# Performance work log

Measured on AMD Instinct MI355X. Metric: run time of the kernel, lower is better.

## Reference

```python
import jax, jax.numpy as jnp
import numpy as np

B, T, D, F, H = 512, 48, 128, 16, 512


def setup_inputs() -> dict:
    key = jax.random.key(0)
    ks = jax.random.split(key, 7)
    return {
        "input": jax.random.normal(ks[0], (B, T, D, F), dtype=jnp.float32),
        "attn_w": jax.random.normal(ks[1], (2 * H + F * T,), dtype=jnp.float32) * 0.02,
        "attn_b": jax.random.normal(ks[2], (1,), dtype=jnp.float32) * 0.02,
        "w_ih": jax.random.normal(ks[3], (4 * H, D * F), dtype=jnp.float32) * 0.02,
        "w_hh": jax.random.normal(ks[4], (4 * H, H), dtype=jnp.float32) * 0.02,
        "b_ih": jax.random.normal(ks[5], (4 * H,), dtype=jnp.float32) * 0.02,
        "b_hh": jax.random.normal(ks[6], (4 * H,), dtype=jnp.float32) * 0.02,
    }


def reference(input, attn_w, attn_b, w_ih, w_hh, b_ih, b_hh):
    Bsz, Ts, Dn, Fn = input.shape
    Hs = w_hh.shape[1]
    # permute(0,2,3,1): [B, T, D, F] -> [B, D, F, T]
    x_perm = jnp.transpose(input, (0, 2, 3, 1))
    x_flat = x_perm.reshape(Bsz, Dn, Fn * Ts)  # [B, D, F*T]
    # encode_attn input is concat(hidden, cell, x); split the weight accordingly
    w_h, w_c, w_x = attn_w[:Hs], attn_w[Hs:2 * Hs], attn_w[2 * Hs:]
    # x contribution to attention logits is constant across steps
    e_x = x_flat @ w_x + attn_b[0]             # [B, D]
    xs = jnp.moveaxis(x_perm, 3, 0)            # [T, B, D, F] (time-major for scan)
    bias = b_ih + b_hh                         # fuse the two LSTM biases

    def step(carry, x_t):
        h, c = carry                           # [B, H] each
        e = e_x + (h @ w_h)[:, None] + (c @ w_c)[:, None]  # [B, D]
        a = jax.nn.softmax(e, axis=-1)
        x_hat = (a[:, :, None] * x_t).reshape(Bsz, Dn * Fn)  # [B, D*F]
        gates = x_hat @ w_ih.T + h @ w_hh.T + bias            # [B, 4H]
        i, f, g, o = jnp.split(gates, 4, axis=-1)  # torch LSTM gate order
        c_new = jax.nn.sigmoid(f) * c + jax.nn.sigmoid(i) * jnp.tanh(g)
        h_new = jax.nn.sigmoid(o) * jnp.tanh(c_new)
        return (h_new, c_new), h_new

    h0 = jnp.zeros((Bsz, Hs), dtype=input.dtype)
    _, hs = jax.lax.scan(step, (h0, h0), xs)   # hs: [T, B, H]
    return jnp.transpose(hs, (1, 0, 2))        # [B, T, H] == hidden_states[:, 1:]
```

## Files before the change

kernel.cpp:

```cpp
#include <hip/hip_runtime.h>

#define B_ 512
#define T_ 48
#define D_ 128
#define F_ 16
#define H_ 512

typedef float f32x4 __attribute__((ext_vector_type(4)));
typedef short s16x8 __attribute__((ext_vector_type(8)));
typedef unsigned short u16x8 __attribute__((ext_vector_type(8)));
typedef unsigned short u16x4 __attribute__((ext_vector_type(4)));
typedef unsigned long long u64;

__device__ __forceinline__ unsigned short f2bf(float x) {
  unsigned u = __float_as_uint(x);
  u += 0x7fffu + ((u >> 16) & 1u);
  return (unsigned short)(u >> 16);
}
__device__ __forceinline__ float bf2f(unsigned short h) {
  return __uint_as_float(((unsigned)h) << 16);
}
__device__ __forceinline__ float sigmoidf_(float x) {
  return 1.f / (1.f + expf(-x));
}

__device__ __forceinline__ void st_sys_u64(u64* p, u64 v) {
  __hip_atomic_store(p, v, __ATOMIC_RELAXED, __HIP_MEMORY_SCOPE_SYSTEM);
}
__device__ __forceinline__ u64 ld_sys_u64(const u64* p) {
  return __hip_atomic_load((u64*)p, __ATOMIC_RELAXED, __HIP_MEMORY_SCOPE_SYSTEM);
}
__device__ __forceinline__ void st_sys_u32(unsigned* p, unsigned v) {
  __hip_atomic_store(p, v, __ATOMIC_RELAXED, __HIP_MEMORY_SCOPE_SYSTEM);
}
__device__ __forceinline__ unsigned ld_sys_u32(const unsigned* p) {
  return __hip_atomic_load((unsigned*)p, __ATOMIC_RELAXED, __HIP_MEMORY_SCOPE_SYSTEM);
}

#define AS1 __attribute__((address_space(1)))
#define AS3 __attribute__((address_space(3)))
__device__ __forceinline__ void g2lds16(const void* g, void* l) {
  __builtin_amdgcn_global_load_lds((const AS1 void*)g, (AS3 void*)l, 16, 0, 0);
}

__global__ __launch_bounds__(256) void k_prep(const float* __restrict__ wih,
                                              const float* __restrict__ whh,
                                              unsigned short* __restrict__ wih_b,
                                              unsigned short* __restrict__ whh_b) {
  long i4 = ((long)blockIdx.x * 256 + threadIdx.x) * 4;
  if (i4 < 4194304) {
    float4 v = *(const float4*)(wih + i4);
    u16x4 o = {f2bf(v.x), f2bf(v.y), f2bf(v.z), f2bf(v.w)};
    *(u16x4*)(wih_b + i4) = o;
  } else {
    long j = i4 - 4194304;
    if (j < 1048576) {
      float4 v = *(const float4*)(whh + j);
      u16x4 o = {f2bf(v.x), f2bf(v.y), f2bf(v.z), f2bf(v.w)};
      *(u16x4*)(whh_b + j) = o;
    }
  }
}

__global__ __launch_bounds__(128) void k_ex(const float* __restrict__ in,
                                            const float* __restrict__ attn_w,
                                            const float* __restrict__ attn_b,
                                            float* __restrict__ a_out) {
  __shared__ float wx[768];
  __shared__ float red[128];
  const int b = blockIdx.x, d = threadIdx.x;
  for (int i = d; i < 768; i += 128) wx[i] = attn_w[1024 + i];
  __syncthreads();
  const float* base = in + (long)b * 98304 + (long)d * 16;
  float acc = 0.f;
  for (int t = 0; t < 48; ++t) {
    const float4* p = (const float4*)(base + (long)t * 2048);
    float4 v0 = p[0], v1 = p[1], v2 = p[2], v3 = p[3];
    acc += v0.x * wx[t]       + v0.y * wx[48 + t]  + v0.z * wx[96 + t]  + v0.w * wx[144 + t];
    acc += v1.x * wx[192 + t] + v1.y * wx[240 + t] + v1.z * wx[288 + t] + v1.w * wx[336 + t];
    acc += v2.x * wx[384 + t] + v2.y * wx[432 + t] + v2.z * wx[480 + t] + v2.w * wx[528 + t];
    acc += v3.x * wx[576 + t] + v3.y * wx[624 + t] + v3.z * wx[672 + t] + v3.w * wx[720 + t];
  }
  acc += attn_b[0];
  red[d] = acc;
  __syncthreads();
  for (int s = 64; s > 0; s >>= 1) {
    if (d < s) red[d] = fmaxf(red[d], red[d + s]);
    __syncthreads();
  }
  float mx = red[0];
  __syncthreads();
  float ex = expf(acc - mx);
  red[d] = ex;
  __syncthreads();
  for (int s = 64; s > 0; s >>= 1) {
    if (d < s) red[d] += red[d + s];
    __syncthreads();
  }
  a_out[b * 128 + d] = ex / red[0];
}

__global__ __launch_bounds__(256) void k_xhat(const float* __restrict__ in,
                                              const float* __restrict__ a,
                                              unsigned short* __restrict__ xh) {
  const int mrow = blockIdx.x;
  const int t = mrow >> 9, b = mrow & 511;
  const int tid = threadIdx.x;
  const int k = tid * 8;
  const int d = k >> 4;
  const int f0 = k & 15;
  const float* src = in + (((long)(b * 48 + t) * 128 + d) * 16 + f0);
  float4 v0 = *(const float4*)src;
  float4 v1 = *(const float4*)(src + 4);
  float s = a[b * 128 + d];
  u16x8 o;
  o[0] = f2bf(v0.x * s); o[1] = f2bf(v0.y * s); o[2] = f2bf(v0.z * s); o[3] = f2bf(v0.w * s);
  o[4] = f2bf(v1.x * s); o[5] = f2bf(v1.y * s); o[6] = f2bf(v1.z * s); o[7] = f2bf(v1.w * s);
  *(u16x8*)(xh + (long)mrow * 2048 + k) = o;
}


#define G_STAGE(ktv, s)                                                         \
  do {                                                                          \
    const long ko_ = (long)(ktv) * 64 + (long)(s) * 262144;                     \
    char* la_ = (char*)SM + ((ktv) & 1) * 32768 + (s) * 16384 + ldsw;           \
    g2lds16(Ag + ko_, la_);                                                     \
    g2lds16(Ag + ko_ + 131072, la_ + 8192);                                     \
    g2lds16(Bg + ko_, la_ + 65536);                                             \
    g2lds16(Bg + ko_ + 131072, la_ + 73728);                                    \
  } while (0)

#define G_LDA(bufel, ksv, mh)                                                   \
  do {                                                                          \
    const unsigned short* ab_ =                                                 \
        SM + (bufel) + aBase + (mh) * 4096 + (psw ^ ((ksv) * 32));              \
    af[0] = *(const s16x8*)(ab_);                                               \
    af[1] = *(const s16x8*)(ab_ + 1024);                                        \
    af[2] = *(const s16x8*)(ab_ + 2048);                                        \
    af[3] = *(const s16x8*)(ab_ + 3072);                                        \
  } while (0)

#define G_LDB(bufel, ksv)                                                       \
  do {                                                                          \
    const unsigned short* bb_ = SM + (bufel) + bBase + (psw ^ ((ksv) * 32));    \
    bv[0] = *(const s16x8*)(bb_);                                               \
    bv[1] = *(const s16x8*)(bb_ + 1024);                                        \
    bv[2] = *(const s16x8*)(bb_ + 2048);                                        \
    bv[3] = *(const s16x8*)(bb_ + 3072);                                        \
  } while (0)

#define G_BARW()                                                                \
  do {                                                                          \
    __builtin_amdgcn_s_barrier();                                               \
    asm volatile("s_waitcnt lgkmcnt(0)" ::: "memory");                          \
    __builtin_amdgcn_sched_barrier(0);                                          \
  } while (0)

#define G_MMA(mh)                                                               \
  do {                                                                          \
    __builtin_amdgcn_s_setprio(1);                                              \
    _Pragma("unroll") for (int mt_ = 0; mt_ < 4; ++mt_)                         \
        _Pragma("unroll") for (int nt_ = 0; nt_ < 4; ++nt_)                     \
            acc[(mh) * 4 + mt_][nt_] = __builtin_amdgcn_mfma_f32_16x16x32_bf16( \
                af[mt_], bv[nt_], acc[(mh) * 4 + mt_][nt_], 0, 0, 0);           \
    __builtin_amdgcn_s_setprio(0);                                              \
  } while (0)

#define G_GATE(n) asm volatile("s_waitcnt vmcnt(" #n ")" ::: "memory")

__global__ __launch_bounds__(512, 2) void k_gemm(const unsigned short* __restrict__ A,
                                                 const unsigned short* __restrict__ Bw,
                                                 unsigned short* __restrict__ C) {
  __shared__ __align__(16) unsigned short SM[65536];
  const int tid = threadIdx.x;
  const int w = tid >> 6, lane = tid & 63;
  const int q = lane >> 4, l16 = lane & 15;
  const int wm = w >> 2, wn = w & 3;
  const int id = blockIdx.x;
  const int xcd = id & 7, j = id >> 3;
  const long m0 = ((long)xcd * 12 + (j >> 3)) * 256;
  const long n0 = (long)(j & 7) * 256;

  const int srow = w * 8 + (lane >> 3);
  const int csrc = (lane & 7) ^ (lane >> 3);
  const unsigned short* Ag = A + (m0 + srow) * 2048 + csrc * 8;
  const unsigned short* Bg = Bw + (n0 + srow) * 2048 + csrc * 8;
  const int ldsw = w * 1024;

  const int psw = (q ^ (l16 & 7)) * 8;
  const int aBase = (wm * 128 + l16) * 64;
  const int bBase = 32768 + (wn * 64 + l16) * 64;

  f32x4 acc[8][4];
  const f32x4 zz = {0.f, 0.f, 0.f, 0.f};
#pragma unroll
  for (int i = 0; i < 8; ++i)
#pragma unroll
    for (int j2 = 0; j2 < 4; ++j2) acc[i][j2] = zz;
  s16x8 af[4], bv[4];

  G_STAGE(0, 0);
  G_STAGE(0, 1);
  G_GATE(0);
  __builtin_amdgcn_s_barrier();

#pragma unroll 2
  for (int kt = 0; kt < 31; ++kt) {
    const int bufel = (kt & 1) * 16384;
    G_LDB(bufel, 0); G_LDA(bufel, 0, 0);
    G_STAGE(kt + 1, 0);
    G_BARW(); G_MMA(0);
    __builtin_amdgcn_s_barrier();
    G_LDA(bufel, 0, 1);
    G_STAGE(kt + 1, 1);
    G_BARW(); G_MMA(1);
    __builtin_amdgcn_s_barrier();
    G_LDB(bufel, 1); G_LDA(bufel, 1, 0);
    G_BARW(); G_MMA(0);
    __builtin_amdgcn_s_barrier();
    G_LDA(bufel, 1, 1);
    G_BARW(); G_MMA(1);
    G_GATE(0);
    __builtin_amdgcn_s_barrier();
  }
  {
    G_LDB(16384, 0); G_LDA(16384, 0, 0);
    G_BARW(); G_MMA(0);
    __builtin_amdgcn_s_barrier();
    G_LDA(16384, 0, 1);
    G_BARW(); G_MMA(1);
    __builtin_amdgcn_s_barrier();
    G_LDB(16384, 1); G_LDA(16384, 1, 0);
    G_BARW(); G_MMA(0);
    __builtin_amdgcn_s_barrier();
    G_LDA(16384, 1, 1);
    G_BARW(); G_MMA(1);
  }

#pragma unroll
  for (int mh = 0; mh < 2; ++mh)
#pragma unroll
    for (int mt = 0; mt < 4; ++mt)
#pragma unroll
      for (int nt = 0; nt < 4; ++nt)
#pragma unroll
        for (int r = 0; r < 4; ++r) {
          long m = m0 + wm * 128 + mh * 64 + mt * 16 + q * 4 + r;
          long n = n0 + wn * 64 + nt * 16 + l16;
          C[m * 2048 + n] = f2bf(acc[mh * 4 + mt][nt][r]);
        }
}

__global__ __launch_bounds__(256, 1) void k_rec(const unsigned short* __restrict__ gx,
                                                const unsigned short* __restrict__ whh_b,
                                                const float* __restrict__ b_ih,
                                                const float* __restrict__ b_hh,
                                                unsigned short* __restrict__ h_buf,
                                                float* __restrict__ out,
                                                unsigned int* __restrict__ bar) {
  __shared__ unsigned short hs[32 * 528];
  __shared__ float gsm[4 * 32 * 36];
  const int tid = threadIdx.x;
  const int wave = tid >> 6, lane = tid & 63;
  const int q = lane >> 4, l16 = lane & 15;
  const int bt = blockIdx.x & 15, g = blockIdx.x >> 4;
  const int b0 = bt * 32;
  const int pm = tid >> 3, pr = (tid & 7) * 4;
  const int srow = tid >> 3, st7 = tid & 7;
  unsigned int* slots = &bar[bt * 16];

  s16x8 wreg[32];
#pragma unroll
  for (int nt = 0; nt < 2; ++nt) {
    const unsigned short* wp = whh_b + (long)(wave * 512 + g * 32 + nt * 16 + l16) * 512 + q * 8;
#pragma unroll
    for (int kk = 0; kk < 16; ++kk)
      wreg[nt * 16 + kk] = *(const s16x8*)(wp + kk * 32);
  }
#pragma unroll
  for (int i = 0; i < 32; ++i) asm volatile("" : "+v"(wreg[i]));

  float bias_[16];
#pragma unroll
  for (int qq = 0; qq < 4; ++qq)
#pragma unroll
    for (int rr = 0; rr < 4; ++rr) {
      int j = qq * 512 + g * 32 + pr + rr;
      bias_[qq * 4 + rr] = b_ih[j] + b_hh[j];
    }
  float creg[4] = {0.f, 0.f, 0.f, 0.f};
  const f32x4 zz = {0.f, 0.f, 0.f, 0.f};

  for (int t = 0; t < 48; ++t) {
    u16x4 gxr[4];
    const unsigned short* gp = gx + ((long)t * 512 + b0 + pm) * 2048 + g * 32 + pr;
#pragma unroll
    for (int qq = 0; qq < 4; ++qq) gxr[qq] = *(const u16x4*)(gp + qq * 512);

    f32x4 acc[2][2] = {{zz, zz}, {zz, zz}};
    if (t > 0) {
      if (wave == 0 && lane < 16) {
        while (ld_sys_u32(&slots[lane]) < (unsigned)t)
          __builtin_amdgcn_s_sleep(1);
      }
      __syncthreads();
      const u64* hp = (const u64*)(h_buf + ((t - 1) & 1) * (512 * 512) + (long)b0 * 512);
      u64 tmp[16];
#pragma unroll
      for (int j = 0; j < 16; ++j)
        tmp[j] = ld_sys_u64(hp + (long)srow * 128 + st7 + 8 * j);
#pragma unroll
      for (int j = 0; j < 16; ++j)
        *(u64*)&hs[srow * 528 + (st7 + 8 * j) * 4] = tmp[j];
      __syncthreads();
#pragma unroll
      for (int kk = 0; kk < 16; ++kk) {
        s16x8 af0 = *(const s16x8*)&hs[l16 * 528 + kk * 32 + q * 8];
        s16x8 af1 = *(const s16x8*)&hs[(16 + l16) * 528 + kk * 32 + q * 8];
        acc[0][0] = __builtin_amdgcn_mfma_f32_16x16x32_bf16(af0, wreg[kk],      acc[0][0], 0, 0, 0);
        acc[0][1] = __builtin_amdgcn_mfma_f32_16x16x32_bf16(af0, wreg[16 + kk], acc[0][1], 0, 0, 0);
        acc[1][0] = __builtin_amdgcn_mfma_f32_16x16x32_bf16(af1, wreg[kk],      acc[1][0], 0, 0, 0);
        acc[1][1] = __builtin_amdgcn_mfma_f32_16x16x32_bf16(af1, wreg[16 + kk], acc[1][1], 0, 0, 0);
      }
    }
#pragma unroll
    for (int mt = 0; mt < 2; ++mt)
#pragma unroll
      for (int nt = 0; nt < 2; ++nt)
        *(f32x4*)&gsm[(wave * 32 + nt * 16 + l16) * 36 + mt * 16 + q * 4] = acc[mt][nt];
    __syncthreads();
    float hval[4];
#pragma unroll
    for (int rr = 0; rr < 4; ++rr) {
      float gv[4];
#pragma unroll
      for (int qq = 0; qq < 4; ++qq)
        gv[qq] = gsm[(qq * 32 + pr + rr) * 36 + pm] + bf2f(gxr[qq][rr]) + bias_[qq * 4 + rr];
      float is = sigmoidf_(gv[0]);
      float fs = sigmoidf_(gv[1]);
      float gt = tanhf(gv[2]);
      float os = sigmoidf_(gv[3]);
      creg[rr] = fs * creg[rr] + is * gt;
      hval[rr] = os * tanhf(creg[rr]);
    }
    u16x4 hb = {f2bf(hval[0]), f2bf(hval[1]), f2bf(hval[2]), f2bf(hval[3])};
    u64 hb8;
    __builtin_memcpy(&hb8, &hb, 8);
    st_sys_u64((u64*)&h_buf[(t & 1) * (512 * 512) + (b0 + pm) * 512 + g * 32 + pr], hb8);
    f32x4 ov = {hval[0], hval[1], hval[2], hval[3]};
    __builtin_nontemporal_store(ov, (f32x4*)&out[(long)(b0 + pm) * (T_ * H_) + (long)t * H_ + g * 32 + pr]);
    __syncthreads();
    if (t < 47 && tid == 0)
      st_sys_u32(&slots[g], (unsigned)(t + 1));
  }
}

extern "C" void kernel_launch(void* const* d_in, const int* in_sizes, int n_in,
                              void* d_out, int out_size, void* d_ws, size_t ws_size,
                              hipStream_t stream) {
  const float* input  = (const float*)d_in[0];
  const float* attn_w = (const float*)d_in[1];
  const float* attn_b = (const float*)d_in[2];
  const float* w_ih   = (const float*)d_in[3];
  const float* w_hh   = (const float*)d_in[4];
  const float* b_ih   = (const float*)d_in[5];
  const float* b_hh   = (const float*)d_in[6];
  float* out = (float*)d_out;

  char* ws = (char*)d_ws;
  unsigned int* bar     = (unsigned int*)ws;
  float* a_ws           = (float*)(ws + 1024);
  unsigned short* h_buf = (unsigned short*)(ws + 263168);
  unsigned short* whh_b = (unsigned short*)(ws + 1311744);
  unsigned short* wih_b = (unsigned short*)(ws + 3408896);
  unsigned short* x_hat = (unsigned short*)(ws + 11797504);
  unsigned short* gxws  = (unsigned short*)(ws + 112460800);

  (void)hipMemsetAsync(d_ws, 0, 1024, stream);
  hipLaunchKernelGGL(k_prep, dim3(5120), dim3(256), 0, stream, w_ih, w_hh, wih_b, whh_b);
  hipLaunchKernelGGL(k_ex, dim3(512), dim3(128), 0, stream, input, attn_w, attn_b, a_ws);
  hipLaunchKernelGGL(k_xhat, dim3(24576), dim3(256), 0, stream, input, a_ws, x_hat);
  hipLaunchKernelGGL(k_gemm, dim3(768), dim3(512), 0, stream, x_hat, wih_b, gxws);
  hipLaunchKernelGGL(k_rec, dim3(256), dim3(256), 0, stream, gxws, whh_b, b_ih, b_hh, h_buf, out, bar);
}
```

Baseline: 722.6 us.

## Drop intra-iteration barriers in GEMM K-loop, repad LDS, and signal before output store

The GEMM main loop now loads all A/B fragments for a K-tile into separate register sets and interleaves the LDS reads with the MFMA groups. This removes the three barrier-plus-lgkmcnt waits per iteration, so reads and matrix math can overlap. In the recurrent kernel, the LDS padding for the hidden-state tile and gate scratch is changed (528→520, 36→37) to alter bank-conflict patterns. The output store is moved after the cross-block step signal so dependent blocks are released earlier. The extra fragment registers raise register pressure and could cause spills. The 37-float stride makes the 16-byte vector LDS stores misaligned.

```diff
diff --git a/kernel.cpp b/kernel.cpp
--- a/kernel.cpp
+++ b/kernel.cpp
@@ -130,39 +130,32 @@
     g2lds16(Bg + ko_ + 131072, la_ + 73728);                                    \
   } while (0)
 
-#define G_LDA(bufel, ksv, mh)                                                   \
+#define G_LDA4(dst, bufel, ksv, mh)                                             \
   do {                                                                          \
     const unsigned short* ab_ =                                                 \
         SM + (bufel) + aBase + (mh) * 4096 + (psw ^ ((ksv) * 32));              \
-    af[0] = *(const s16x8*)(ab_);                                               \
-    af[1] = *(const s16x8*)(ab_ + 1024);                                        \
-    af[2] = *(const s16x8*)(ab_ + 2048);                                        \
-    af[3] = *(const s16x8*)(ab_ + 3072);                                        \
+    dst[0] = *(const s16x8*)(ab_);                                              \
+    dst[1] = *(const s16x8*)(ab_ + 1024);                                       \
+    dst[2] = *(const s16x8*)(ab_ + 2048);                                       \
+    dst[3] = *(const s16x8*)(ab_ + 3072);                                       \
   } while (0)
 
-#define G_LDB(bufel, ksv)                                                       \
+#define G_LDB4(dst, bufel, ksv)                                                 \
   do {                                                                          \
     const unsigned short* bb_ = SM + (bufel) + bBase + (psw ^ ((ksv) * 32));    \
-    bv[0] = *(const s16x8*)(bb_);                                               \
-    bv[1] = *(const s16x8*)(bb_ + 1024);                                        \
-    bv[2] = *(const s16x8*)(bb_ + 2048);                                        \
-    bv[3] = *(const s16x8*)(bb_ + 3072);                                        \
+    dst[0] = *(const s16x8*)(bb_);                                              \
+    dst[1] = *(const s16x8*)(bb_ + 1024);                                       \
+    dst[2] = *(const s16x8*)(bb_ + 2048);                                       \
+    dst[3] = *(const s16x8*)(bb_ + 3072);                                       \
   } while (0)
 
-#define G_BARW()                                                                \
-  do {                                                                          \
-    __builtin_amdgcn_s_barrier();                                               \
-    asm volatile("s_waitcnt lgkmcnt(0)" ::: "memory");                          \
-    __builtin_amdgcn_sched_barrier(0);                                          \
-  } while (0)
-
-#define G_MMA(mh)                                                               \
+#define G_MMA2(mh, Af, Bf)                                                      \
   do {                                                                          \
     __builtin_amdgcn_s_setprio(1);                                              \
     _Pragma("unroll") for (int mt_ = 0; mt_ < 4; ++mt_)                         \
         _Pragma("unroll") for (int nt_ = 0; nt_ < 4; ++nt_)                     \
             acc[(mh) * 4 + mt_][nt_] = __builtin_amdgcn_mfma_f32_16x16x32_bf16( \
-                af[mt_], bv[nt_], acc[(mh) * 4 + mt_][nt_], 0, 0, 0);           \
+                Af[mt_], Bf[nt_], acc[(mh) * 4 + mt_][nt_], 0, 0, 0);           \
     __builtin_amdgcn_s_setprio(0);                                              \
   } while (0)
 
@@ -197,44 +190,43 @@
   for (int i = 0; i < 8; ++i)
 #pragma unroll
     for (int j2 = 0; j2 < 4; ++j2) acc[i][j2] = zz;
-  s16x8 af[4], bv[4];
 
   G_STAGE(0, 0);
   G_STAGE(0, 1);
   G_GATE(0);
   __builtin_amdgcn_s_barrier();
 
-#pragma unroll 2
+#pragma unroll 1
   for (int kt = 0; kt < 31; ++kt) {
     const int bufel = (kt & 1) * 16384;
-    G_LDB(bufel, 0); G_LDA(bufel, 0, 0);
+    s16x8 b0[4], b1[4], a00[4], a01[4], a10[4], a11[4];
+    G_LDB4(b0, bufel, 0);
+    G_LDA4(a00, bufel, 0, 0);
     G_STAGE(kt + 1, 0);
-    G_BARW(); G_MMA(0);
-    __builtin_amdgcn_s_barrier();
-    G_LDA(bufel, 0, 1);
+    G_LDA4(a01, bufel, 0, 1);
     G_STAGE(kt + 1, 1);
-    G_BARW(); G_MMA(1);
-    __builtin_amdgcn_s_barrier();
-    G_LDB(bufel, 1); G_LDA(bufel, 1, 0);
-    G_BARW(); G_MMA(0);
-    __builtin_amdgcn_s_barrier();
-    G_LDA(bufel, 1, 1);
-    G_BARW(); G_MMA(1);
+    G_MMA2(0, a00, b0);
+    G_LDB4(b1, bufel, 1);
+    G_LDA4(a10, bufel, 1, 0);
+    G_MMA2(1, a01, b0);
+    G_LDA4(a11, bufel, 1, 1);
+    G_MMA2(0, a10, b1);
+    G_MMA2(1, a11, b1);
     G_GATE(0);
     __builtin_amdgcn_s_barrier();
   }
   {
-    G_LDB(16384, 0); G_LDA(16384, 0, 0);
-    G_BARW(); G_MMA(0);
-    __builtin_amdgcn_s_barrier();
-    G_LDA(16384, 0, 1);
-    G_BARW(); G_MMA(1);
-    __builtin_amdgcn_s_barrier();
-    G_LDB(16384, 1); G_LDA(16384, 1, 0);
-    G_BARW(); G_MMA(0);
-    __builtin_amdgcn_s_barrier();
-    G_LDA(16384, 1, 1);
-    G_BARW(); G_MMA(1);
+    s16x8 b0[4], b1[4], a00[4], a01[4], a10[4], a11[4];
+    G_LDB4(b0, 16384, 0);
+    G_LDA4(a00, 16384, 0, 0);
+    G_LDA4(a01, 16384, 0, 1);
+    G_MMA2(0, a00, b0);
+    G_LDB4(b1, 16384, 1);
+    G_LDA4(a10, 16384, 1, 0);
+    G_MMA2(1, a01, b0);
+    G_LDA4(a11, 16384, 1, 1);
+    G_MMA2(0, a10, b1);
+    G_MMA2(1, a11, b1);
   }
 
 #pragma unroll
@@ -258,8 +250,8 @@
                                                 unsigned short* __restrict__ h_buf,
                                                 float* __restrict__ out,
                                                 unsigned int* __restrict__ bar) {
-  __shared__ unsigned short hs[32 * 528];
-  __shared__ float gsm[4 * 32 * 36];
+  __shared__ unsigned short hs[32 * 520];
+  __shared__ float gsm[4 * 32 * 37];
   const int tid = threadIdx.x;
   const int wave = tid >> 6, lane = tid & 63;
   const int q = lane >> 4, l16 = lane & 15;
@@ -311,12 +303,12 @@
         tmp[j] = ld_sys_u64(hp + (long)srow * 128 + st7 + 8 * j);
 #pragma unroll
       for (int j = 0; j < 16; ++j)
-        *(u64*)&hs[srow * 528 + (st7 + 8 * j) * 4] = tmp[j];
+        *(u64*)&hs[srow * 520 + (st7 + 8 * j) * 4] = tmp[j];
       __syncthreads();
 #pragma unroll
       for (int kk = 0; kk < 16; ++kk) {
-        s16x8 af0 = *(const s16x8*)&hs[l16 * 528 + kk * 32 + q * 8];
-        s16x8 af1 = *(const s16x8*)&hs[(16 + l16) * 528 + kk * 32 + q * 8];
+        s16x8 af0 = *(const s16x8*)&hs[l16 * 520 + kk * 32 + q * 8];
+        s16x8 af1 = *(const s16x8*)&hs[(16 + l16) * 520 + kk * 32 + q * 8];
         acc[0][0] = __builtin_amdgcn_mfma_f32_16x16x32_bf16(af0, wreg[kk],      acc[0][0], 0, 0, 0);
         acc[0][1] = __builtin_amdgcn_mfma_f32_16x16x32_bf16(af0, wreg[16 + kk], acc[0][1], 0, 0, 0);
         acc[1][0] = __builtin_amdgcn_mfma_f32_16x16x32_bf16(af1, wreg[kk],      acc[1][0], 0, 0, 0);
@@ -327,7 +319,7 @@
     for (int mt = 0; mt < 2; ++mt)
 #pragma unroll
       for (int nt = 0; nt < 2; ++nt)
-        *(f32x4*)&gsm[(wave * 32 + nt * 16 + l16) * 36 + mt * 16 + q * 4] = acc[mt][nt];
+        *(f32x4*)&gsm[(wave * 32 + nt * 16 + l16) * 37 + mt * 16 + q * 4] = acc[mt][nt];
     __syncthreads();
     float hval[4];
 #pragma unroll
@@ -335,7 +327,7 @@
       float gv[4];
 #pragma unroll
       for (int qq = 0; qq < 4; ++qq)
-        gv[qq] = gsm[(qq * 32 + pr + rr) * 36 + pm] + bf2f(gxr[qq][rr]) + bias_[qq * 4 + rr];
+        gv[qq] = gsm[(qq * 32 + pr + rr) * 37 + pm] + bf2f(gxr[qq][rr]) + bias_[qq * 4 + rr];
       float is = sigmoidf_(gv[0]);
       float fs = sigmoidf_(gv[1]);
       float gt = tanhf(gv[2]);
@@ -347,11 +339,11 @@
     u64 hb8;
     __builtin_memcpy(&hb8, &hb, 8);
     st_sys_u64((u64*)&h_buf[(t & 1) * (512 * 512) + (b0 + pm) * 512 + g * 32 + pr], hb8);
-    f32x4 ov = {hval[0], hval[1], hval[2], hval[3]};
-    __builtin_nontemporal_store(ov, (f32x4*)&out[(long)(b0 + pm) * (T_ * H_) + (long)t * H_ + g * 32 + pr]);
     __syncthreads();
     if (t < 47 && tid == 0)
       st_sys_u32(&slots[g], (unsigned)(t + 1));
+    f32x4 ov = {hval[0], hval[1], hval[2], hval[3]};
+    __builtin_nontemporal_store(ov, (f32x4*)&out[(long)(b0 + pm) * (T_ * H_) + (long)t * H_ + g * 32 + pr]);
   }
 }
 
```

Measured after the change: 718.4 us. No clear change (-0.6%).
